# Kernel tuning notes

Measured on AMD Instinct MI355X. Metric: run time of the kernel, lower is better.

The kernel has to match this reference:

```python
import jax, jax.numpy as jnp
import numpy as np

N_HEADS = 8
HEAD_DIM = 32
GROUPS = 32
EPS = 1e-5


def setup_inputs() -> dict:
    key = jax.random.key(0)
    ks = jax.random.split(key, 3)
    b, c, h, w = 8, 256, 32, 32
    x = jax.random.normal(ks[0], (b, c, h, w), dtype=jnp.float32)
    norm_w = jnp.ones((c,), dtype=jnp.float32)
    norm_b = jnp.zeros((c,), dtype=jnp.float32)
    qkv_w = jax.random.normal(ks[1], (3 * c, c), dtype=jnp.float32) * (c ** -0.5)
    qkv_b = jnp.zeros((3 * c,), dtype=jnp.float32)
    out_w = jax.random.normal(ks[2], (c, c), dtype=jnp.float32) * (c ** -0.5)
    out_b = jnp.zeros((c,), dtype=jnp.float32)
    return {"x": x, "norm_w": norm_w, "norm_b": norm_b,
            "qkv_w": qkv_w, "qkv_b": qkv_b, "out_w": out_w, "out_b": out_b}


def _group_norm(x, weight, bias):
    b, c, h, w = x.shape
    xr = x.reshape(b, GROUPS, -1)  # [b, 32, (c//32)*h*w]
    mu = xr.mean(axis=-1, keepdims=True)
    var = xr.var(axis=-1, keepdims=True)
    xn = ((xr - mu) * jax.lax.rsqrt(var + EPS)).reshape(b, c, h, w)
    return xn * weight[:, None, None] + bias[:, None, None]


def _conv1x1(x, w, b):
    # 1x1 conv == channel matmul
    return jnp.einsum('oc,bchw->bohw', w, x) + b[None, :, None, None]


def reference(x, norm_w, norm_b, qkv_w, qkv_b, out_w, out_b):
    b, c, h, w = x.shape
    hw = h * w
    scale = HEAD_DIM ** (-0.5)
    qkv = _conv1x1(_group_norm(x, norm_w, norm_b), qkv_w, qkv_b)  # [b, 3c, h, w]
    q, k, v = jnp.split(qkv, 3, axis=1)
    # torch reshape(b, n_heads, c//n_heads, h*w) is a raw row-major reshape
    q = q.reshape(b, N_HEADS, HEAD_DIM, hw) * scale
    k = k.reshape(b, N_HEADS, HEAD_DIM, hw)
    v = v.reshape(b, N_HEADS, HEAD_DIM, hw)
    sim = jnp.einsum('bhdi,bhdj->bhij', q, k)  # [b, heads, hw, hw]
    sim = sim - jax.lax.stop_gradient(sim.max(axis=-1, keepdims=True))
    attn = jax.nn.softmax(sim, axis=-1)
    out = jnp.einsum('bhij,bhdj->bhid', attn, v)  # [b, heads, hw, head_dim]
    # faithful to the original: raw reshape (b, heads, hw, head_dim) -> (b, c, h, w)
    out = out.reshape(b, c, h, w)
    return _conv1x1(out, out_w, out_b) + x
```

## Files before the change

kernel.cpp:

```cpp
#include <hip/hip_runtime.h>
#include <hip/hip_bf16.h>

#define NB 8
#define NC 256
#define NHW 1024

typedef unsigned short u16;
typedef unsigned int u32;
using f16x8  = __attribute__((ext_vector_type(8))) _Float16;
using f32x16 = __attribute__((ext_vector_type(16))) float;
using u32x4  = __attribute__((ext_vector_type(4))) unsigned int;
using u16x8  = __attribute__((ext_vector_type(8))) unsigned short;

static __device__ inline u16 f2h(float f) {
    _Float16 h = (_Float16)f;
    return __builtin_bit_cast(u16, h);
}
static __device__ inline float h2f(u16 u) {
    return (float)__builtin_bit_cast(_Float16, u);
}
static __device__ inline unsigned pk2(float a, float b) {
    auto r = __builtin_amdgcn_cvt_pkrtz(a, b);
    return __builtin_bit_cast(unsigned, r);
}
static __device__ inline void gload16(const void* g, void* l) {
    __builtin_amdgcn_global_load_lds(
        (const __attribute__((address_space(1))) void*)g,
        (__attribute__((address_space(3))) void*)l, 16, 0, 0);
}
static __device__ inline float vmax16(const f32x16& v) {
    float m0 = fmaxf(fmaxf(v[0], v[1]), fmaxf(v[2], v[3]));
    float m1 = fmaxf(fmaxf(v[4], v[5]), fmaxf(v[6], v[7]));
    float m2 = fmaxf(fmaxf(v[8], v[9]), fmaxf(v[10], v[11]));
    float m3 = fmaxf(fmaxf(v[12], v[13]), fmaxf(v[14], v[15]));
    return fmaxf(fmaxf(m0, m1), fmaxf(m2, m3));
}
static __device__ inline float vsum16(const f32x16& v) {
    float s0 = (v[0] + v[1]) + (v[2] + v[3]);
    float s1 = (v[4] + v[5]) + (v[6] + v[7]);
    float s2 = (v[8] + v[9]) + (v[10] + v[11]);
    float s3 = (v[12] + v[13]) + (v[14] + v[15]);
    return (s0 + s1) + (s2 + s3);
}
template<int B>
static __device__ inline f16x8 packP(const f32x16& p, const int h) {
    unsigned u0 = pk2(p[B + 0], p[B + 1]);
    unsigned u1 = pk2(p[B + 2], p[B + 3]);
    unsigned u2 = pk2(p[B + 4], p[B + 5]);
    unsigned u3 = pk2(p[B + 6], p[B + 7]);
    unsigned pu0 = __shfl_xor(u0, 32);
    unsigned pu1 = __shfl_xor(u1, 32);
    unsigned pu2 = __shfl_xor(u2, 32);
    unsigned pu3 = __shfl_xor(u3, 32);
    u32x4 w;
    w[0] = h ? pu2 : u0;
    w[1] = h ? pu3 : u1;
    w[2] = h ? u2 : pu0;
    w[3] = h ? u3 : pu1;
    return __builtin_bit_cast(f16x8, w);
}

__global__ __launch_bounds__(256) void prep_kernel(
    const float* __restrict__ x, const float* __restrict__ qkv_w,
    const float* __restrict__ out_w, float2* __restrict__ stats,
    u16* __restrict__ Wq, u16* __restrict__ Wo)
{
    __shared__ float rs[4][2];
    const int bid = blockIdx.x, t = threadIdx.x;
    if (bid < 256) {
        const int g = bid & 31, b = bid >> 5;
        const size_t base = ((size_t)b * NC + g * 8) * NHW;
        const float4* xi = (const float4*)(x + base);
        float sum = 0.f, sq = 0.f;
#pragma unroll
        for (int i = 0; i < 8; ++i) {
            float4 v = xi[t + i * 256];
            sum += v.x + v.y + v.z + v.w;
            sq += v.x * v.x + v.y * v.y + v.z * v.z + v.w * v.w;
        }
        const int lane = t & 63, wv = t >> 6;
#pragma unroll
        for (int o = 32; o > 0; o >>= 1) {
            sum += __shfl_down(sum, o, 64);
            sq += __shfl_down(sq, o, 64);
        }
        if (lane == 0) { rs[wv][0] = sum; rs[wv][1] = sq; }
        __syncthreads();
        if (t == 0) {
            float S = rs[0][0] + rs[1][0] + rs[2][0] + rs[3][0];
            float Q = rs[0][1] + rs[1][1] + rs[2][1] + rs[3][1];
            float mu = S * (1.f / 8192.f);
            float var = Q * (1.f / 8192.f) - mu * mu;
            stats[b * 32 + g] = make_float2(mu, rsqrtf(var + 1e-5f));
        }
    } else {
        const int f4 = (bid - 256) * 256 + t;
        float4 v;
        u16* dhp;
        int e;
        if (f4 < 49152) {
            e = f4 * 4;
            v = *(const float4*)&qkv_w[e];
            if ((e >> 8) < 256) {
                const float s = 0.17677669529663687f;
                v.x *= s; v.y *= s; v.z *= s; v.w *= s;
            }
            dhp = Wq;
        } else {
            e = (f4 - 49152) * 4;
            v = *(const float4*)&out_w[e];
            dhp = Wo;
        }
        ushort4 hh;
        hh.x = f2h(v.x); hh.y = f2h(v.y); hh.z = f2h(v.z); hh.w = f2h(v.w);
        *(ushort4*)&dhp[e] = hh;
    }
}

__global__ __launch_bounds__(256) void tsplit_kernel(
    const float* __restrict__ src, const float2* __restrict__ stats,
    const float* __restrict__ gw, const float* __restrict__ gb,
    u16* __restrict__ dh)
{
    __shared__ float lds[64][68];
    const int b = blockIdx.z;
    const int c0 = blockIdx.y * 64, hw0 = blockIdx.x * 64;
    const int t = threadIdx.x;
    const int cL = t >> 4, hwL = (t & 15) * 4;
#pragma unroll
    for (int i = 0; i < 4; ++i) {
        const int c = c0 + cL + i * 16;
        float4 v = *(const float4*)&src[((size_t)b * 256 + c) * 1024 + hw0 + hwL];
        const float2 st = stats[b * 32 + (c >> 3)];
        const float sc = gw[c] * st.y;
        const float off = gb[c] - st.x * sc;
        v.x = v.x * sc + off; v.y = v.y * sc + off;
        v.z = v.z * sc + off; v.w = v.w * sc + off;
        *(float4*)&lds[cL + i * 16][hwL] = v;
    }
    __syncthreads();
    const int lane = t & 63, w = t >> 6;
    const int hwR = lane, cq = w * 16;
    u16x8 H0, H1;
#pragma unroll
    for (int j = 0; j < 8; ++j) {
        H0[j] = f2h(lds[cq + j][hwR]);
        H1[j] = f2h(lds[cq + 8 + j][hwR]);
    }
    const size_t o = ((size_t)b * 1024 + hw0 + hwR) * 256 + c0 + cq;
    *(u16x8*)&dh[o] = H0; *(u16x8*)&dh[o + 8] = H1;
}

__global__ __launch_bounds__(256) void qkv_gemm_kernel(
    const u16* __restrict__ W, const u16* __restrict__ B,
    const float* __restrict__ bias,
    u16* __restrict__ qT, u16* __restrict__ kT, u16* __restrict__ vN)
{
    __shared__ __align__(16) u16 sB[2][2048];
    const int b = blockIdx.z;
    const int m0 = blockIdx.y * 128, n0 = blockIdx.x * 64;
    const int t = threadIdx.x, w = t >> 6, lane = t & 63;
    const int l31 = lane & 31, h = lane >> 5;
    const int msub = m0 + w * 32;

    const u16* Bb = B + ((size_t)b * 1024 + n0) * 256;
    const u16* War = W + (size_t)(msub + l31) * 256 + h * 8;

    const float bscale = (msub < 256) ? 0.17677669529663687f : 1.0f;
    f32x16 acc[2];
#pragma unroll
    for (int r = 0; r < 16; ++r) {
        const int crow = (r & 3) + 8 * (r >> 2) + 4 * h;
        const float bv = bias[msub + crow] * bscale;
        acc[0][r] = bv; acc[1][r] = bv;
    }

    const int srow = (t >> 2) & 63;
    const int sg = (t & 3) ^ (srow & 3);
    const u16* sh0 = Bb + (size_t)srow * 256 + sg * 8;
    const int wseg = w * 512;

    gload16(sh0, &sB[0][wseg]);
    __syncthreads();
    int cur = 0;
    for (int kc = 0; kc < 8; ++kc) {
        if (kc < 7) {
            gload16(sh0 + (kc + 1) * 32, &sB[cur ^ 1][wseg]);
        }
#pragma unroll
        for (int k16 = 0; k16 < 2; ++k16) {
            const f16x8 ah = *(const f16x8*)(War + kc * 32 + k16 * 16);
            const int gi = ((k16 * 2 + h) ^ (l31 & 3)) * 8;
#pragma unroll
            for (int ns = 0; ns < 2; ++ns) {
                const int row = ns * 32 + l31;
                const f16x8 bh = *(const f16x8*)&sB[cur][row * 32 + gi];
                acc[ns] = __builtin_amdgcn_mfma_f32_32x32x16_f16(ah, bh, acc[ns], 0, 0, 0);
            }
        }
        __syncthreads();
        cur ^= 1;
    }

    const int type = msub >> 8;
    const int head = (msub >> 5) & 7;
    const int bh_ = b * 8 + head;
    if (type < 2) {
        u16* dst = type ? kT : qT;
#pragma unroll
        for (int ns = 0; ns < 2; ++ns) {
            const int n = n0 + ns * 32 + l31;
            u16* p = dst + ((size_t)bh_ * 1024 + n) * 32;
#pragma unroll
            for (int rp = 0; rp < 8; ++rp) {
                const int r = rp * 2;
                const int d = (r & 3) + 8 * (r >> 2) + 4 * h;
                *(unsigned*)&p[d] = (unsigned)f2h(acc[ns][r]) | ((unsigned)f2h(acc[ns][r + 1]) << 16);
            }
        }
    } else {
#pragma unroll
        for (int ns = 0; ns < 2; ++ns) {
            const int n = n0 + ns * 32 + l31;
#pragma unroll
            for (int r = 0; r < 16; ++r) {
                const int d = (r & 3) + 8 * (r >> 2) + 4 * h;
                vN[((size_t)bh_ * 32 + d) * 1024 + n] = f2h(acc[ns][r]);
            }
        }
    }
}

__global__ __launch_bounds__(256) void attn_mfma_kernel(
    const u16* __restrict__ qT, const u16* __restrict__ kT,
    const u16* __restrict__ vN, u16* __restrict__ ao)
{
    __shared__ __align__(16) u16 Ks[2][2048];
    __shared__ __align__(16) u16 Vs[2][2048];
    const int bid = blockIdx.x;
    const int itile = bid >> 6, bh = bid & 63;
    const int b = bh >> 3, head = bh & 7;
    const int t = threadIdx.x;
    const int lane = t & 63;
    const int w = t >> 6;
    const int l31 = lane & 31;
    const int h = lane >> 5;
    const int ibase = itile * 128 + w * 32;

    const u16* qrow = qT + ((size_t)bh * 1024 + ibase + l31) * 32;
    const f16x8 qf0 = *(const f16x8*)(qrow + h * 8);
    const f16x8 qf1 = *(const f16x8*)(qrow + 16 + h * 8);

    f32x16 out = {};
    float m = -1e30f, lsum = 0.f;

    const u16* ksrc = kT + ((size_t)bh * 1024 + (t >> 2)) * 32 + ((t & 3) ^ ((t >> 2) & 3)) * 8;
    const u16* vsrc = vN + ((size_t)bh * 32 + (t >> 3)) * 1024 + ((t & 7) ^ ((t >> 3) & 7)) * 8;
    const int wseg = w * 512;

    gload16(ksrc, &Ks[0][wseg]);
    gload16(vsrc, &Vs[0][wseg]);
    __syncthreads();
    int cur = 0;
    for (int T = 0; T < 16; ++T) {
        if (T < 15) {
            gload16(ksrc + (size_t)(T + 1) * 2048, &Ks[cur ^ 1][wseg]);
            gload16(vsrc + (T + 1) * 64, &Vs[cur ^ 1][wseg]);
        }
        const int gk0 = (h ^ (l31 & 3)) * 8;
        const int gk1 = ((2 + h) ^ (l31 & 3)) * 8;
        const f16x8 kf00 = *(const f16x8*)&Ks[cur][l31 * 32 + gk0];
        const f16x8 kf01 = *(const f16x8*)&Ks[cur][l31 * 32 + gk1];
        const f16x8 kf10 = *(const f16x8*)&Ks[cur][(32 + l31) * 32 + gk0];
        const f16x8 kf11 = *(const f16x8*)&Ks[cur][(32 + l31) * 32 + gk1];
        f32x16 sA = {}, sB = {};
        sA = __builtin_amdgcn_mfma_f32_32x32x16_f16(kf00, qf0, sA, 0, 0, 0);
        sA = __builtin_amdgcn_mfma_f32_32x32x16_f16(kf01, qf1, sA, 0, 0, 0);
        sB = __builtin_amdgcn_mfma_f32_32x32x16_f16(kf10, qf0, sB, 0, 0, 0);
        sB = __builtin_amdgcn_mfma_f32_32x32x16_f16(kf11, qf1, sB, 0, 0, 0);

        float mt = fmaxf(vmax16(sA), vmax16(sB));
        mt = fmaxf(mt, __shfl_xor(mt, 32));
        if (!__all(mt <= m + 8.f)) {
            const float mn = fmaxf(m, mt);
            const float cor = __expf(m - mn);
            m = mn;
            lsum *= cor;
#pragma unroll
            for (int r = 0; r < 16; ++r) {
                const int src = (r & 3) + 8 * (r >> 2) + 4 * h;
                out[r] *= __shfl(cor, src);
            }
        }
#pragma unroll
        for (int r = 0; r < 16; ++r) {
            sA[r] = __expf(sA[r] - m);
            sB[r] = __expf(sB[r] - m);
        }
        float ps = vsum16(sA) + vsum16(sB);
        ps += __shfl_xor(ps, 32);
        lsum += ps;

        const f16x8 pf0 = packP<0>(sA, h);
        const f16x8 pf1 = packP<8>(sA, h);
        const f16x8 pf2 = packP<0>(sB, h);
        const f16x8 pf3 = packP<8>(sB, h);
        const int vx = l31 & 7;
        const f16x8 vf0 = *(const f16x8*)&Vs[cur][l31 * 64 + ((h    ) ^ vx) * 8];
        const f16x8 vf1 = *(const f16x8*)&Vs[cur][l31 * 64 + ((2 + h) ^ vx) * 8];
        const f16x8 vf2 = *(const f16x8*)&Vs[cur][l31 * 64 + ((4 + h) ^ vx) * 8];
        const f16x8 vf3 = *(const f16x8*)&Vs[cur][l31 * 64 + ((6 + h) ^ vx) * 8];
        out = __builtin_amdgcn_mfma_f32_32x32x16_f16(pf0, vf0, out, 0, 0, 0);
        out = __builtin_amdgcn_mfma_f32_32x32x16_f16(pf1, vf1, out, 0, 0, 0);
        out = __builtin_amdgcn_mfma_f32_32x32x16_f16(pf2, vf2, out, 0, 0, 0);
        out = __builtin_amdgcn_mfma_f32_32x32x16_f16(pf3, vf3, out, 0, 0, 0);
        __syncthreads();
        cur ^= 1;
    }

    const float linv = 1.f / lsum;
    const int cOut = b * 256 + head * 32 + itile * 4 + w;
    u16* og = ao + (size_t)cOut * 1024 + l31;
#pragma unroll
    for (int r = 0; r < 16; ++r) {
        const int crow = (r & 3) + 8 * (r >> 2) + 4 * h;
        const float sc = __shfl(linv, crow);
        og[crow * 32] = f2h(out[r] * sc);
    }
}

__global__ __launch_bounds__(256) void out_gemm_kernel(
    const u16* __restrict__ W, const u16* __restrict__ ao,
    const float* __restrict__ bias,
    const float* __restrict__ res, float* __restrict__ Y)
{
    __shared__ __align__(16) u16 sB[2][2048];
    const int b = blockIdx.z;
    const int m0 = blockIdx.y * 64, n0 = blockIdx.x * 64;
    const int t = threadIdx.x, w = t >> 6, lane = t & 63;
    const int l31 = lane & 31, h = lane >> 5;
    const int wm = w >> 1, wn = w & 1;
    const int msub = m0 + wm * 32;

    const u16* War = W + (size_t)(msub + l31) * 256 + h * 8;

    f32x16 acc;
#pragma unroll
    for (int r = 0; r < 16; ++r) {
        const int crow = (r & 3) + 8 * (r >> 2) + 4 * h;
        acc[r] = bias[msub + crow];
    }

    const int kL = t >> 3, pb = (t & 7) * 8;
    const u16* asrc = ao + ((size_t)b * 256 + kL) * 1024 + n0 + pb;
    u16x8 regs;

#define LOADC(kc) { regs = *(const u16x8*)(asrc + (size_t)(kc) * 32 * 1024); }
#define WRITEC(buf) { _Pragma("unroll") for (int e = 0; e < 8; ++e) { \
        const int n = pb + e; \
        const int idx = n * 32 + ((kL >> 3) ^ (n & 3)) * 8 + (kL & 7); \
        sB[buf][idx] = regs[e]; } }

    LOADC(0); WRITEC(0);
    __syncthreads();
    int cur = 0;
    for (int kc = 0; kc < 8; ++kc) {
        if (kc < 7) LOADC(kc + 1);
#pragma unroll
        for (int k16 = 0; k16 < 2; ++k16) {
            const f16x8 ah = *(const f16x8*)(War + kc * 32 + k16 * 16);
            const int gi = ((k16 * 2 + h) ^ (l31 & 3)) * 8;
            const int row = wn * 32 + l31;
            const f16x8 bh = *(const f16x8*)&sB[cur][row * 32 + gi];
            acc = __builtin_amdgcn_mfma_f32_32x32x16_f16(ah, bh, acc, 0, 0, 0);
        }
        if (kc < 7) WRITEC(cur ^ 1);
        __syncthreads();
        cur ^= 1;
    }
    const int n = n0 + wn * 32 + l31;
#pragma unroll
    for (int r = 0; r < 16; ++r) {
        const int mm = msub + (r & 3) + 8 * (r >> 2) + 4 * h;
        const size_t idx = ((size_t)b * 256 + mm) * 1024 + n;
        Y[idx] = acc[r] + res[idx];
    }
#undef LOADC
#undef WRITEC
}

extern "C" void kernel_launch(void* const* d_in, const int* in_sizes, int n_in,
                              void* d_out, int out_size, void* d_ws, size_t ws_size,
                              hipStream_t stream) {
    const float* x      = (const float*)d_in[0];
    const float* norm_w = (const float*)d_in[1];
    const float* norm_b = (const float*)d_in[2];
    const float* qkv_w  = (const float*)d_in[3];
    const float* qkv_b  = (const float*)d_in[4];
    const float* out_w  = (const float*)d_in[5];
    const float* out_b  = (const float*)d_in[6];
    float* out = (float*)d_out;

    char* p = (char*)d_ws;
    float2* stats = (float2*)p;  p += 4096;
    u16* XT  = (u16*)p;  p += 4u * 1024 * 1024;
    u16* Wq  = (u16*)p;  p += 393216 * 2;
    u16* Wo  = (u16*)p;  p += 131072 * 2;
    u16* qT  = (u16*)p;  p += 4u * 1024 * 1024;
    u16* kT  = (u16*)p;  p += 4u * 1024 * 1024;
    u16* vN  = (u16*)p;  p += 4u * 1024 * 1024;
    u16* ao  = (u16*)p;  p += 4u * 1024 * 1024;

    prep_kernel<<<512, 256, 0, stream>>>(x, qkv_w, out_w, stats, Wq, Wo);
    tsplit_kernel<<<dim3(16, 4, NB), 256, 0, stream>>>(x, stats, norm_w, norm_b, XT);
    qkv_gemm_kernel<<<dim3(16, 6, NB), 256, 0, stream>>>(Wq, XT, qkv_b, qT, kT, vN);
    attn_mfma_kernel<<<512, 256, 0, stream>>>(qT, kT, vN, ao);
    out_gemm_kernel<<<dim3(16, 4, NB), 256, 0, stream>>>(Wo, ao, out_b, x, out);
}
```

Before: 62.26 us.

## Fuse group-norm transpose into QKV GEMM and fold log2e into Q scale

Removes the separate tsplit kernel: the QKV GEMM now loads fp32 x directly, applies group-norm scale/offset, packs to fp16, and stages into LDS with a new swizzle, overlapping global loads with MFMA. This eliminates a kernel launch and the round-trip of the fp16 transposed activation buffer. Separately, the query scale is premultiplied by log2(e) so the softmax can use exp2f instead of __expf. The trade is that each of the six M-tiles per batch re-reads and re-normalizes x in fp32, and the global reads are strided column loads rather than the earlier contiguous 16-byte loads.

```diff
diff --git a/kernel.cpp b/kernel.cpp
--- a/kernel.cpp
+++ b/kernel.cpp
@@ -60,6 +60,8 @@
     return __builtin_bit_cast(f16x8, w);
 }
 
+#define QSCALE 0.25505412f
+
 __global__ __launch_bounds__(256) void prep_kernel(
     const float* __restrict__ x, const float* __restrict__ qkv_w,
     const float* __restrict__ out_w, float2* __restrict__ stats,
@@ -102,8 +104,7 @@
             e = f4 * 4;
             v = *(const float4*)&qkv_w[e];
             if ((e >> 8) < 256) {
-                const float s = 0.17677669529663687f;
-                v.x *= s; v.y *= s; v.z *= s; v.w *= s;
+                v.x *= QSCALE; v.y *= QSCALE; v.z *= QSCALE; v.w *= QSCALE;
             }
             dhp = Wq;
         } else {
@@ -117,42 +118,10 @@
     }
 }
 
-__global__ __launch_bounds__(256) void tsplit_kernel(
-    const float* __restrict__ src, const float2* __restrict__ stats,
+__global__ __launch_bounds__(256) void qkv_gemm_kernel(
+    const u16* __restrict__ W, const float* __restrict__ x,
+    const float2* __restrict__ stats,
     const float* __restrict__ gw, const float* __restrict__ gb,
-    u16* __restrict__ dh)
-{
-    __shared__ float lds[64][68];
-    const int b = blockIdx.z;
-    const int c0 = blockIdx.y * 64, hw0 = blockIdx.x * 64;
-    const int t = threadIdx.x;
-    const int cL = t >> 4, hwL = (t & 15) * 4;
-#pragma unroll
-    for (int i = 0; i < 4; ++i) {
-        const int c = c0 + cL + i * 16;
-        float4 v = *(const float4*)&src[((size_t)b * 256 + c) * 1024 + hw0 + hwL];
-        const float2 st = stats[b * 32 + (c >> 3)];
-        const float sc = gw[c] * st.y;
-        const float off = gb[c] - st.x * sc;
-        v.x = v.x * sc + off; v.y = v.y * sc + off;
-        v.z = v.z * sc + off; v.w = v.w * sc + off;
-        *(float4*)&lds[cL + i * 16][hwL] = v;
-    }
-    __syncthreads();
-    const int lane = t & 63, w = t >> 6;
-    const int hwR = lane, cq = w * 16;
-    u16x8 H0, H1;
-#pragma unroll
-    for (int j = 0; j < 8; ++j) {
-        H0[j] = f2h(lds[cq + j][hwR]);
-        H1[j] = f2h(lds[cq + 8 + j][hwR]);
-    }
-    const size_t o = ((size_t)b * 1024 + hw0 + hwR) * 256 + c0 + cq;
-    *(u16x8*)&dh[o] = H0; *(u16x8*)&dh[o + 8] = H1;
-}
-
-__global__ __launch_bounds__(256) void qkv_gemm_kernel(
-    const u16* __restrict__ W, const u16* __restrict__ B,
     const float* __restrict__ bias,
     u16* __restrict__ qT, u16* __restrict__ kT, u16* __restrict__ vN)
 {
@@ -163,10 +132,9 @@
     const int l31 = lane & 31, h = lane >> 5;
     const int msub = m0 + w * 32;
 
-    const u16* Bb = B + ((size_t)b * 1024 + n0) * 256;
     const u16* War = W + (size_t)(msub + l31) * 256 + h * 8;
 
-    const float bscale = (msub < 256) ? 0.17677669529663687f : 1.0f;
+    const float bscale = (msub < 256) ? QSCALE : 1.0f;
     f32x16 acc[2];
 #pragma unroll
     for (int r = 0; r < 16; ++r) {
@@ -175,32 +143,49 @@
         acc[0][r] = bv; acc[1][r] = bv;
     }
 
-    const int srow = (t >> 2) & 63;
-    const int sg = (t & 3) ^ (srow & 3);
-    const u16* sh0 = Bb + (size_t)srow * 256 + sg * 8;
-    const int wseg = w * 512;
-
-    gload16(sh0, &sB[0][wseg]);
+    const int sn = t & 63;
+    const int sw = w;
+    const float* xs = x + (size_t)b * 256 * 1024 + (size_t)(sw * 8) * 1024 + n0 + sn;
+    float vreg[8];
+    const int woff = sn * 32 + ((sw ^ ((sn >> 1) & 3)) * 8);
+
+#define LOADX(kcn) { _Pragma("unroll") for (int j = 0; j < 8; ++j) \
+        vreg[j] = xs[(size_t)((kcn) * 32 + j) * 1024]; }
+#define STAGE(kcn, buf) { \
+        const int cb = (kcn) * 32 + sw * 8; \
+        const float2 st = stats[b * 32 + (cb >> 3)]; \
+        u32x4 pkv; \
+        _Pragma("unroll") for (int jp = 0; jp < 4; ++jp) { \
+            const float sc0 = gw[cb + jp * 2] * st.y; \
+            const float of0 = gb[cb + jp * 2] - st.x * sc0; \
+            const float sc1 = gw[cb + jp * 2 + 1] * st.y; \
+            const float of1 = gb[cb + jp * 2 + 1] - st.x * sc1; \
+            pkv[jp] = pk2(vreg[jp * 2] * sc0 + of0, vreg[jp * 2 + 1] * sc1 + of1); } \
+        *(u32x4*)&sB[buf][woff] = pkv; }
+
+    LOADX(0);
+    STAGE(0, 0);
     __syncthreads();
     int cur = 0;
     for (int kc = 0; kc < 8; ++kc) {
-        if (kc < 7) {
-            gload16(sh0 + (kc + 1) * 32, &sB[cur ^ 1][wseg]);
-        }
+        if (kc < 7) LOADX(kc + 1);
 #pragma unroll
         for (int k16 = 0; k16 < 2; ++k16) {
             const f16x8 ah = *(const f16x8*)(War + kc * 32 + k16 * 16);
-            const int gi = ((k16 * 2 + h) ^ (l31 & 3)) * 8;
 #pragma unroll
             for (int ns = 0; ns < 2; ++ns) {
                 const int row = ns * 32 + l31;
+                const int gi = ((k16 * 2 + h) ^ ((row >> 1) & 3)) * 8;
                 const f16x8 bh = *(const f16x8*)&sB[cur][row * 32 + gi];
                 acc[ns] = __builtin_amdgcn_mfma_f32_32x32x16_f16(ah, bh, acc[ns], 0, 0, 0);
             }
         }
+        if (kc < 7) STAGE(kc + 1, cur ^ 1);
         __syncthreads();
         cur ^= 1;
     }
+#undef LOADX
+#undef STAGE
 
     const int type = msub >> 8;
     const int head = (msub >> 5) & 7;
@@ -283,7 +268,7 @@
         mt = fmaxf(mt, __shfl_xor(mt, 32));
         if (!__all(mt <= m + 8.f)) {
             const float mn = fmaxf(m, mt);
-            const float cor = __expf(m - mn);
+            const float cor = exp2f(m - mn);
             m = mn;
             lsum *= cor;
 #pragma unroll
@@ -294,8 +279,8 @@
         }
 #pragma unroll
         for (int r = 0; r < 16; ++r) {
-            sA[r] = __expf(sA[r] - m);
-            sB[r] = __expf(sB[r] - m);
+            sA[r] = exp2f(sA[r] - m);
+            sB[r] = exp2f(sB[r] - m);
         }
         float ps = vsum16(sA) + vsum16(sB);
         ps += __shfl_xor(ps, 32);
@@ -403,7 +388,6 @@
 
     char* p = (char*)d_ws;
     float2* stats = (float2*)p;  p += 4096;
-    u16* XT  = (u16*)p;  p += 4u * 1024 * 1024;
     u16* Wq  = (u16*)p;  p += 393216 * 2;
     u16* Wo  = (u16*)p;  p += 131072 * 2;
     u16* qT  = (u16*)p;  p += 4u * 1024 * 1024;
@@ -412,8 +396,7 @@
     u16* ao  = (u16*)p;  p += 4u * 1024 * 1024;
 
     prep_kernel<<<512, 256, 0, stream>>>(x, qkv_w, out_w, stats, Wq, Wo);
-    tsplit_kernel<<<dim3(16, 4, NB), 256, 0, stream>>>(x, stats, norm_w, norm_b, XT);
-    qkv_gemm_kernel<<<dim3(16, 6, NB), 256, 0, stream>>>(Wq, XT, qkv_b, qT, kT, vN);
+    qkv_gemm_kernel<<<dim3(16, 6, NB), 256, 0, stream>>>(Wq, x, stats, norm_w, norm_b, qkv_b, qT, kT, vN);
     attn_mfma_kernel<<<512, 256, 0, stream>>>(qT, kT, vN, ao);
     out_gemm_kernel<<<dim3(16, 4, NB), 256, 0, stream>>>(Wo, ao, out_b, x, out);
 }
```

Measured after the change: 67.66 us. 8.7% more time.
